# Kernel tuning notes

Hardware: AMD Instinct MI355X
Metric: run time of the kernel (lower is better)

Reference implementation:

```python
import jax, jax.numpy as jnp
import numpy as np

STRIDE = 8
EPS = 1e-7


def decode_bbox(reg, stride):
    # reg: [B, 4, H, W] = (l, t, r, b) distances in stride units.
    B, _, H, W = reg.shape
    cx = (jnp.arange(W, dtype=reg.dtype) + 0.5) * stride  # [W]
    cy = (jnp.arange(H, dtype=reg.dtype) + 0.5) * stride  # [H]
    cx = cx[None, None, :]  # [1,1,W]
    cy = cy[None, :, None]  # [1,H,1]
    l, t, r, b = reg[:, 0], reg[:, 1], reg[:, 2], reg[:, 3]  # each [B,H,W]
    x1 = cx - l * stride
    y1 = cy - t * stride
    x2 = cx + r * stride
    y2 = cy + b * stride
    return jnp.stack([x1, y1, x2, y2], axis=-1)  # [B,H,W,4] xyxy


def bbox_iou_ciou(pred, target):
    # pred, target: [..., 4] xyxy
    px1, py1, px2, py2 = pred[..., 0], pred[..., 1], pred[..., 2], pred[..., 3]
    tx1, ty1, tx2, ty2 = target[..., 0], target[..., 1], target[..., 2], target[..., 3]
    w1, h1 = px2 - px1, py2 - py1
    w2, h2 = tx2 - tx1, ty2 - ty1
    inter = jnp.clip(jnp.minimum(px2, tx2) - jnp.maximum(px1, tx1), 0) * \
            jnp.clip(jnp.minimum(py2, ty2) - jnp.maximum(py1, ty1), 0)
    union = w1 * h1 + w2 * h2 - inter + EPS
    iou = inter / union
    # enclosing box diagonal
    cw = jnp.maximum(px2, tx2) - jnp.minimum(px1, tx1)
    ch = jnp.maximum(py2, ty2) - jnp.minimum(py1, ty1)
    c2 = cw * cw + ch * ch + EPS
    # squared center distance
    rho2 = ((tx1 + tx2 - px1 - px2) ** 2 + (ty1 + ty2 - py1 - py2) ** 2) * 0.25
    # aspect-ratio consistency term
    four_over_pi2 = 4.0 / (np.pi ** 2)
    v = four_over_pi2 * (jnp.arctan(w2 / (h2 + EPS)) - jnp.arctan(w1 / (h1 + EPS))) ** 2
    alpha = jax.lax.stop_gradient(v / (v - iou + (1.0 + EPS)))
    return iou - rho2 / c2 - alpha * v


def setup_inputs() -> dict:
    key = jax.random.key(0)
    k1, k2, k3 = jax.random.split(key, 3)
    B, H, W = 64, 192, 192
    pred_reg = jax.random.uniform(k1, (B, 4, H, W), dtype=jnp.float32) * 4.0
    target_reg = jax.random.uniform(k2, (B, 4, H, W), dtype=jnp.float32) * 4.0
    mask = jax.random.randint(k3, (B, 1, H, W), 0, 2).astype(jnp.bool_)
    return {"pred_reg": pred_reg, "target_reg": target_reg, "mask": mask}


def reference(pred_reg, target_reg, mask):
    m = mask[:, 0].astype(pred_reg.dtype)  # [B,H,W]
    pred_boxes = decode_bbox(pred_reg, STRIDE)      # [B,H,W,4]
    target_boxes = decode_bbox(target_reg, STRIDE)  # [B,H,W,4]
    ciou = bbox_iou_ciou(pred_boxes, target_boxes)  # [B,H,W]
    msum = jnp.sum(m)
    # masked mean over positive anchors; returns 0 when mask is empty
    loss = jnp.sum((1.0 - ciou) * m) / jnp.maximum(msum, 1.0)
    return loss
```

## Files before the change

### kernel.cpp

```cpp
#include <hip/hip_runtime.h>
#include <hip/hip_bf16.h>
#include <math.h>

#define STRIDE_F 8.0f
#define EPS_F 1e-7f
#define PI_2_F 1.57079632679489662f

__device__ __forceinline__ float frcp(float x) { return __builtin_amdgcn_rcpf(x); }

__device__ __forceinline__ float fast_atan_ratio(float w, float h)
{
    float num = fminf(w, h);
    float den = fmaxf(w, h);
    float z   = num * frcp(den);
    float z2  = z * z;
    float p = fmaf(z2, -0.0117212f,  0.05265332f);
    p = fmaf(z2, p, -0.11643287f);
    p = fmaf(z2, p,  0.19354346f);
    p = fmaf(z2, p, -0.33262347f);
    p = fmaf(z2, p,  0.99997726f);
    p = z * p;
    return (w > h) ? (PI_2_F - p) : p;
}

__device__ __forceinline__ void ciou_elem(
    float cx, float cy,
    float pl, float pt, float pr, float pb,
    float tl, float tt, float tr, float tb,
    int m_i, float& ls, float& ms)
{
    float px1 = cx - pl * STRIDE_F;
    float py1 = cy - pt * STRIDE_F;
    float px2 = cx + pr * STRIDE_F;
    float py2 = cy + pb * STRIDE_F;
    float tx1 = cx - tl * STRIDE_F;
    float ty1 = cy - tt * STRIDE_F;
    float tx2 = cx + tr * STRIDE_F;
    float ty2 = cy + tb * STRIDE_F;

    float w1 = px2 - px1, h1 = py2 - py1;
    float w2 = tx2 - tx1, h2 = ty2 - ty1;
    float iw = fmaxf(fminf(px2, tx2) - fmaxf(px1, tx1), 0.0f);
    float ih = fmaxf(fminf(py2, ty2) - fmaxf(py1, ty1), 0.0f);
    float inter = iw * ih;
    float uni   = w1 * h1 + w2 * h2 - inter + EPS_F;
    float iou   = inter * frcp(uni);

    float cw = fmaxf(px2, tx2) - fminf(px1, tx1);
    float ch = fmaxf(py2, ty2) - fminf(py1, ty1);
    float c2 = cw * cw + ch * ch + EPS_F;

    float dx = tx1 + tx2 - px1 - px2;
    float dy = ty1 + ty2 - py1 - py2;
    float rho2 = (dx * dx + dy * dy) * 0.25f;

    const float FOUR_OVER_PI2 = 0.40528473456935109f;
    float dv = fast_atan_ratio(w2, h2 + EPS_F) - fast_atan_ratio(w1, h1 + EPS_F);
    float v  = FOUR_OVER_PI2 * dv * dv;
    float alpha = v * frcp(v - iou + (1.0f + EPS_F));
    float ciou  = iou - rho2 * frcp(c2) - alpha * v;

    float m = (m_i != 0) ? 1.0f : 0.0f;
    ls += (1.0f - ciou) * m;
    ms += m;
}

__global__ __launch_bounds__(256) void ciou_loss_kernel(
    const float4* __restrict__ pred, const float4* __restrict__ tgt,
    const int4* __restrict__ mask, float2* __restrict__ parts,
    int HW4, int W4)
{
    int idx4 = blockIdx.x * blockDim.x + threadIdx.x;
    int bb  = idx4 / HW4;
    int hw4 = idx4 - bb * HW4;
    int h   = hw4 / W4;
    int w4  = hw4 - h * W4;

    float cy = ((float)h + 0.5f) * STRIDE_F;
    float cx0 = ((float)(w4 * 4) + 0.5f) * STRIDE_F;

    size_t base = (size_t)bb * 4 * (size_t)HW4 + (size_t)hw4;
    float4 pl4 = pred[base];
    float4 pt4 = pred[base + (size_t)HW4];
    float4 pr4 = pred[base + 2 * (size_t)HW4];
    float4 pb4 = pred[base + 3 * (size_t)HW4];
    float4 tl4 = tgt[base];
    float4 tt4 = tgt[base + (size_t)HW4];
    float4 tr4 = tgt[base + 2 * (size_t)HW4];
    float4 tb4 = tgt[base + 3 * (size_t)HW4];
    int4   mk4 = mask[idx4];

    float ls = 0.0f, ms = 0.0f;
    ciou_elem(cx0 + 0.0f * STRIDE_F, cy, pl4.x, pt4.x, pr4.x, pb4.x,
              tl4.x, tt4.x, tr4.x, tb4.x, mk4.x, ls, ms);
    ciou_elem(cx0 + 1.0f * STRIDE_F, cy, pl4.y, pt4.y, pr4.y, pb4.y,
              tl4.y, tt4.y, tr4.y, tb4.y, mk4.y, ls, ms);
    ciou_elem(cx0 + 2.0f * STRIDE_F, cy, pl4.z, pt4.z, pr4.z, pb4.z,
              tl4.z, tt4.z, tr4.z, tb4.z, mk4.z, ls, ms);
    ciou_elem(cx0 + 3.0f * STRIDE_F, cy, pl4.w, pt4.w, pr4.w, pb4.w,
              tl4.w, tt4.w, tr4.w, tb4.w, mk4.w, ls, ms);

    #pragma unroll
    for (int off = 32; off > 0; off >>= 1) {
        ls += __shfl_down(ls, off, 64);
        ms += __shfl_down(ms, off, 64);
    }
    __shared__ float s_l[4];
    __shared__ float s_m[4];
    int wave = threadIdx.x >> 6;
    int lane = threadIdx.x & 63;
    if (lane == 0) { s_l[wave] = ls; s_m[wave] = ms; }
    __syncthreads();
    if (threadIdx.x == 0) {
        float2 p;
        p.x = s_l[0] + s_l[1] + s_l[2] + s_l[3];
        p.y = s_m[0] + s_m[1] + s_m[2] + s_m[3];
        parts[blockIdx.x] = p;
    }
}

__global__ __launch_bounds__(256) void reduce_kernel(
    const float2* __restrict__ parts, int n, float* __restrict__ out)
{
    float ls = 0.0f, ms = 0.0f;
    for (int i = threadIdx.x; i < n; i += 256) {
        float2 p = parts[i];
        ls += p.x;
        ms += p.y;
    }
    #pragma unroll
    for (int off = 32; off > 0; off >>= 1) {
        ls += __shfl_down(ls, off, 64);
        ms += __shfl_down(ms, off, 64);
    }
    __shared__ float s_l[4];
    __shared__ float s_m[4];
    int wave = threadIdx.x >> 6;
    int lane = threadIdx.x & 63;
    if (lane == 0) { s_l[wave] = ls; s_m[wave] = ms; }
    __syncthreads();
    if (threadIdx.x == 0) {
        float tls = s_l[0] + s_l[1] + s_l[2] + s_l[3];
        float tms = s_m[0] + s_m[1] + s_m[2] + s_m[3];
        out[0] = tls / fmaxf(tms, 1.0f);
    }
}

extern "C" void kernel_launch(void* const* d_in, const int* in_sizes, int n_in,
                              void* d_out, int out_size, void* d_ws, size_t ws_size,
                              hipStream_t stream) {
    const float4* pred = (const float4*)d_in[0];
    const float4* tgt  = (const float4*)d_in[1];
    const int4*   mask = (const int4*)d_in[2];
    float* out  = (float*)d_out;
    float2* parts = (float2*)d_ws;

    const int B = 64, H = 192, W = 192;
    const int HW = H * W;
    const int total4 = B * HW / 4;
    const int threads = 256;
    const int blocks = total4 / threads;

    ciou_loss_kernel<<<blocks, threads, 0, stream>>>(pred, tgt, mask, parts,
                                                     HW / 4, W / 4);
    reduce_kernel<<<1, threads, 0, stream>>>(parts, blocks, out);
}
```

Measured before the change: 106.2 us.

## Fuse final reduction via last-block ticket and process eight elements per thread

```diff
diff --git a/kernel.cpp b/kernel.cpp
--- a/kernel.cpp
+++ b/kernel.cpp
@@ -5,6 +5,8 @@
 #define STRIDE_F 8.0f
 #define EPS_F 1e-7f
 #define PI_2_F 1.57079632679489662f
+
+#define NBLOCKS 1152
 
 __device__ __forceinline__ float frcp(float x) { return __builtin_amdgcn_rcpf(x); }
 
@@ -68,37 +70,61 @@
 __global__ __launch_bounds__(256) void ciou_loss_kernel(
     const float4* __restrict__ pred, const float4* __restrict__ tgt,
     const int4* __restrict__ mask, float2* __restrict__ parts,
-    int HW4, int W4)
+    unsigned int* __restrict__ ticket, float* __restrict__ out)
 {
-    int idx4 = blockIdx.x * blockDim.x + threadIdx.x;
-    int bb  = idx4 / HW4;
-    int hw4 = idx4 - bb * HW4;
-    int h   = hw4 / W4;
-    int w4  = hw4 - h * W4;
+    const int HW4 = 9216;
+    const int W4  = 48;
+    const int HW8 = 4608;
+    const int W8  = 24;
 
-    float cy = ((float)h + 0.5f) * STRIDE_F;
-    float cx0 = ((float)(w4 * 4) + 0.5f) * STRIDE_F;
+    int idx8 = blockIdx.x * blockDim.x + threadIdx.x;
+    int bb  = idx8 / HW8;
+    int hw8 = idx8 - bb * HW8;
+    int h   = hw8 / W8;
+    int w8  = hw8 - h * W8;
 
-    size_t base = (size_t)bb * 4 * (size_t)HW4 + (size_t)hw4;
-    float4 pl4 = pred[base];
-    float4 pt4 = pred[base + (size_t)HW4];
-    float4 pr4 = pred[base + 2 * (size_t)HW4];
-    float4 pb4 = pred[base + 3 * (size_t)HW4];
-    float4 tl4 = tgt[base];
-    float4 tt4 = tgt[base + (size_t)HW4];
-    float4 tr4 = tgt[base + 2 * (size_t)HW4];
-    float4 tb4 = tgt[base + 3 * (size_t)HW4];
-    int4   mk4 = mask[idx4];
+    float cy  = ((float)h + 0.5f) * STRIDE_F;
+    float cx0 = ((float)(w8 * 8) + 0.5f) * STRIDE_F;
+
+    size_t base4 = (size_t)bb * 4 * HW4 + (size_t)h * W4 + (size_t)w8 * 2;
+    size_t m4    = (size_t)bb * HW4 + (size_t)h * W4 + (size_t)w8 * 2;
+
+    float4 pl4a = pred[base4];
+    float4 pl4b = pred[base4 + 1];
+    float4 pt4a = pred[base4 + HW4];
+    float4 pt4b = pred[base4 + HW4 + 1];
+    float4 pr4a = pred[base4 + 2 * HW4];
+    float4 pr4b = pred[base4 + 2 * HW4 + 1];
+    float4 pb4a = pred[base4 + 3 * HW4];
+    float4 pb4b = pred[base4 + 3 * HW4 + 1];
+    float4 tl4a = tgt[base4];
+    float4 tl4b = tgt[base4 + 1];
+    float4 tt4a = tgt[base4 + HW4];
+    float4 tt4b = tgt[base4 + HW4 + 1];
+    float4 tr4a = tgt[base4 + 2 * HW4];
+    float4 tr4b = tgt[base4 + 2 * HW4 + 1];
+    float4 tb4a = tgt[base4 + 3 * HW4];
+    float4 tb4b = tgt[base4 + 3 * HW4 + 1];
+    int4   mka  = mask[m4];
+    int4   mkb  = mask[m4 + 1];
 
     float ls = 0.0f, ms = 0.0f;
-    ciou_elem(cx0 + 0.0f * STRIDE_F, cy, pl4.x, pt4.x, pr4.x, pb4.x,
-              tl4.x, tt4.x, tr4.x, tb4.x, mk4.x, ls, ms);
-    ciou_elem(cx0 + 1.0f * STRIDE_F, cy, pl4.y, pt4.y, pr4.y, pb4.y,
-              tl4.y, tt4.y, tr4.y, tb4.y, mk4.y, ls, ms);
-    ciou_elem(cx0 + 2.0f * STRIDE_F, cy, pl4.z, pt4.z, pr4.z, pb4.z,
-              tl4.z, tt4.z, tr4.z, tb4.z, mk4.z, ls, ms);
-    ciou_elem(cx0 + 3.0f * STRIDE_F, cy, pl4.w, pt4.w, pr4.w, pb4.w,
-              tl4.w, tt4.w, tr4.w, tb4.w, mk4.w, ls, ms);
+    ciou_elem(cx0 + 0*STRIDE_F, cy, pl4a.x, pt4a.x, pr4a.x, pb4a.x,
+              tl4a.x, tt4a.x, tr4a.x, tb4a.x, mka.x, ls, ms);
+    ciou_elem(cx0 + 1*STRIDE_F, cy, pl4a.y, pt4a.y, pr4a.y, pb4a.y,
+              tl4a.y, tt4a.y, tr4a.y, tb4a.y, mka.y, ls, ms);
+    ciou_elem(cx0 + 2*STRIDE_F, cy, pl4a.z, pt4a.z, pr4a.z, pb4a.z,
+              tl4a.z, tt4a.z, tr4a.z, tb4a.z, mka.z, ls, ms);
+    ciou_elem(cx0 + 3*STRIDE_F, cy, pl4a.w, pt4a.w, pr4a.w, pb4a.w,
+              tl4a.w, tt4a.w, tr4a.w, tb4a.w, mka.w, ls, ms);
+    ciou_elem(cx0 + 4*STRIDE_F, cy, pl4b.x, pt4b.x, pr4b.x, pb4b.x,
+              tl4b.x, tt4b.x, tr4b.x, tb4b.x, mkb.x, ls, ms);
+    ciou_elem(cx0 + 5*STRIDE_F, cy, pl4b.y, pt4b.y, pr4b.y, pb4b.y,
+              tl4b.y, tt4b.y, tr4b.y, tb4b.y, mkb.y, ls, ms);
+    ciou_elem(cx0 + 6*STRIDE_F, cy, pl4b.z, pt4b.z, pr4b.z, pb4b.z,
+              tl4b.z, tt4b.z, tr4b.z, tb4b.z, mkb.z, ls, ms);
+    ciou_elem(cx0 + 7*STRIDE_F, cy, pl4b.w, pt4b.w, pr4b.w, pb4b.w,
+              tl4b.w, tt4b.w, tr4b.w, tb4b.w, mkb.w, ls, ms);
 
     #pragma unroll
     for (int off = 32; off > 0; off >>= 1) {
@@ -107,6 +133,7 @@
     }
     __shared__ float s_l[4];
     __shared__ float s_m[4];
+    __shared__ bool s_last;
     int wave = threadIdx.x >> 6;
     int lane = threadIdx.x & 63;
     if (lane == 0) { s_l[wave] = ls; s_m[wave] = ms; }
@@ -116,28 +143,31 @@
         p.x = s_l[0] + s_l[1] + s_l[2] + s_l[3];
         p.y = s_m[0] + s_m[1] + s_m[2] + s_m[3];
         parts[blockIdx.x] = p;
+        __threadfence();
+        unsigned int old = atomicAdd(ticket, 1u);
+        s_last = (old == (unsigned int)(NBLOCKS - 1));
     }
-}
+    __syncthreads();
+    if (!s_last) return;
 
-__global__ __launch_bounds__(256) void reduce_kernel(
-    const float2* __restrict__ parts, int n, float* __restrict__ out)
-{
-    float ls = 0.0f, ms = 0.0f;
-    for (int i = threadIdx.x; i < n; i += 256) {
-        float2 p = parts[i];
-        ls += p.x;
-        ms += p.y;
+    __threadfence();
+    float fl = 0.0f, fm = 0.0f;
+    for (int i = threadIdx.x; i < NBLOCKS; i += 256) {
+        unsigned long long u = __hip_atomic_load(
+            (const unsigned long long*)&parts[i],
+            __ATOMIC_RELAXED, __HIP_MEMORY_SCOPE_AGENT);
+        union { unsigned long long u; float2 f; } cvt;
+        cvt.u = u;
+        fl += cvt.f.x;
+        fm += cvt.f.y;
     }
     #pragma unroll
     for (int off = 32; off > 0; off >>= 1) {
-        ls += __shfl_down(ls, off, 64);
-        ms += __shfl_down(ms, off, 64);
+        fl += __shfl_down(fl, off, 64);
+        fm += __shfl_down(fm, off, 64);
     }
-    __shared__ float s_l[4];
-    __shared__ float s_m[4];
-    int wave = threadIdx.x >> 6;
-    int lane = threadIdx.x & 63;
-    if (lane == 0) { s_l[wave] = ls; s_m[wave] = ms; }
+    __syncthreads();
+    if (lane == 0) { s_l[wave] = fl; s_m[wave] = fm; }
     __syncthreads();
     if (threadIdx.x == 0) {
         float tls = s_l[0] + s_l[1] + s_l[2] + s_l[3];
@@ -152,16 +182,12 @@
     const float4* pred = (const float4*)d_in[0];
     const float4* tgt  = (const float4*)d_in[1];
     const int4*   mask = (const int4*)d_in[2];
-    float* out  = (float*)d_out;
+    float* out = (float*)d_out;
+
     float2* parts = (float2*)d_ws;
+    unsigned int* ticket = (unsigned int*)((char*)d_ws + NBLOCKS * sizeof(float2));
 
-    const int B = 64, H = 192, W = 192;
-    const int HW = H * W;
-    const int total4 = B * HW / 4;
-    const int threads = 256;
-    const int blocks = total4 / threads;
+    hipMemsetAsync(ticket, 0, sizeof(unsigned int), stream);
 
-    ciou_loss_kernel<<<blocks, threads, 0, stream>>>(pred, tgt, mask, parts,
-                                                     HW / 4, W / 4);
-    reduce_kernel<<<1, threads, 0, stream>>>(parts, blocks, out);
+    ciou_loss_kernel<<<NBLOCKS, 256, 0, stream>>>(pred, tgt, mask, parts, ticket, out);
 }
```

Result: slower. 156.0 us (+46.9%).
